# Kernel optimization log

Measured on AMD Instinct MI355X. Metric: run time of the kernel, lower is better.

The kernel has to match this reference:

```python
import math
import jax, jax.numpy as jnp
import numpy as np

B, T, E = 1, 4096, 768
H, D = 12, 64
RA_WINDOW = 512
INIT_GATES = (2.2, 0.6, 0.1)


def setup_inputs() -> dict:
    key = jax.random.key(0)
    ks = jax.random.split(key, 6)
    x = jax.random.normal(ks[0], (B, T, E), dtype=jnp.float32)
    # Linear weights stored as [in, out] (math-equivalent to torch's x @ W.T)
    s = 1.0 / math.sqrt(E)
    Wq = jax.random.normal(ks[1], (E, H * D), dtype=jnp.float32) * s
    Wk = jax.random.normal(ks[2], (E, H * D), dtype=jnp.float32) * s
    Wv = jax.random.normal(ks[3], (E, H * D), dtype=jnp.float32) * s
    Wo = jax.random.normal(ks[4], (H * D, E), dtype=jnp.float32) * s
    gates = jnp.tile(jnp.asarray(INIT_GATES, dtype=jnp.float32)[None, :], (H, 1))  # [H,3]
    u = jax.random.normal(ks[5], (H, D), dtype=jnp.float32) * 0.02
    return {"x": x, "Wq": Wq, "Wk": Wk, "Wv": Wv, "Wo": Wo, "gates": gates, "u": u}


def reference(x, Wq, Wk, Wv, Wo, gates, u):
    # projections -> [B,H,T,D]
    def proj(W):
        return (x @ W).reshape(B, T, H, D).transpose(0, 2, 1, 3)
    Q, K, V = proj(Wq), proj(Wk), proj(Wv)

    S = jnp.einsum('bhtd,bhsd->bhts', Q, K) / math.sqrt(D)  # [B,H,T,T]

    w = jax.nn.softmax(gates, axis=-1)  # [H,3]
    w_std = w[:, 0][None, :, None, None]
    w_rec = w[:, 1][None, :, None, None]
    w_disc = w[:, 2][None, :, None, None]

    logits = w_std * S + w_rec * jnp.swapaxes(S, -2, -1)

    # discoverability column bias from K via per-head u
    d_raw = jnp.einsum('bhtd,hd->bht', K, u)
    d = d_raw - jnp.mean(d_raw, axis=-1, keepdims=True)
    logits = logits + w_disc * d[:, :, None, :]

    # causal banded mask
    idx = jnp.arange(T)
    mask = (idx[None, :] <= idx[:, None]) & (jnp.abs(idx[None, :] - idx[:, None]) <= RA_WINDOW)
    logits = jnp.where(mask[None, None, :, :], logits, -jnp.inf)

    attn = jax.nn.softmax(logits, axis=-1)
    ctx = jnp.einsum('bhts,bhsd->bhtd', attn, V)
    out = ctx.transpose(0, 2, 1, 3).reshape(B, T, H * D) @ Wo
    return (out, attn)
```

## Files before the change

### kernel.cpp

```cpp
#include <hip/hip_runtime.h>
#include <cstddef>

#define T_LEN 4096
#define EMB 768
#define NH 12
#define HD 64
#define WIN 512

__global__ __launch_bounds__(256) void gemm_f32_64x64(const float* __restrict__ A,
                                                      const float* __restrict__ B,
                                                      float* __restrict__ C,
                                                      int M, int N, int K) {
    __shared__ float As[16][68];
    __shared__ float Bs[16][68];
    const int tid = threadIdx.x;
    const int bm = blockIdx.y * 64;
    const int bn = blockIdx.x * 64;
    const int tm = (tid >> 4) << 2;
    const int tn = (tid & 15) << 2;

    const int lm  = tid >> 2;
    const int lk  = (tid & 3) << 2;
    const int bkr = tid >> 4;
    const int bnc = (tid & 15) << 2;

    float acc[4][4] = {};

    for (int k0 = 0; k0 < K; k0 += 16) {
        float4 a4 = *(const float4*)&A[(size_t)(bm + lm) * K + k0 + lk];
        As[lk + 0][lm] = a4.x;
        As[lk + 1][lm] = a4.y;
        As[lk + 2][lm] = a4.z;
        As[lk + 3][lm] = a4.w;
        *(float4*)&Bs[bkr][bnc] = *(const float4*)&B[(size_t)(k0 + bkr) * N + bn + bnc];
        __syncthreads();
#pragma unroll
        for (int k = 0; k < 16; ++k) {
            float4 av = *(float4*)&As[k][tm];
            float4 bv = *(float4*)&Bs[k][tn];
            acc[0][0] += av.x * bv.x; acc[0][1] += av.x * bv.y; acc[0][2] += av.x * bv.z; acc[0][3] += av.x * bv.w;
            acc[1][0] += av.y * bv.x; acc[1][1] += av.y * bv.y; acc[1][2] += av.y * bv.z; acc[1][3] += av.y * bv.w;
            acc[2][0] += av.z * bv.x; acc[2][1] += av.z * bv.y; acc[2][2] += av.z * bv.z; acc[2][3] += av.z * bv.w;
            acc[3][0] += av.w * bv.x; acc[3][1] += av.w * bv.y; acc[3][2] += av.w * bv.z; acc[3][3] += av.w * bv.w;
        }
        __syncthreads();
    }
#pragma unroll
    for (int i = 0; i < 4; ++i) {
        float4 cv = make_float4(acc[i][0], acc[i][1], acc[i][2], acc[i][3]);
        *(float4*)&C[(size_t)(bm + tm + i) * N + bn + tn] = cv;
    }
}

__global__ __launch_bounds__(256) void dbias_kernel(const float* __restrict__ K,
                                                    const float* __restrict__ u,
                                                    float* __restrict__ d_bias) {
    const int h = blockIdx.x;
    const int tid = threadIdx.x;
    __shared__ __align__(16) float us[HD];
    __shared__ float dr[T_LEN];
    __shared__ float red[256];
    if (tid < HD) us[tid] = u[h * HD + tid];
    __syncthreads();
    const float4* u4 = (const float4*)us;
    float lsum = 0.f;
    for (int t = tid; t < T_LEN; t += 256) {
        const float4* Kp = (const float4*)&K[(size_t)t * EMB + h * HD];
        float acc = 0.f;
#pragma unroll
        for (int i = 0; i < HD / 4; ++i) {
            float4 k4 = Kp[i];
            float4 uu = u4[i];
            acc += k4.x * uu.x + k4.y * uu.y + k4.z * uu.z + k4.w * uu.w;
        }
        dr[t] = acc;
        lsum += acc;
    }
    red[tid] = lsum;
    __syncthreads();
    for (int off = 128; off > 0; off >>= 1) {
        if (tid < off) red[tid] += red[tid + off];
        __syncthreads();
    }
    const float mean = red[0] * (1.0f / (float)T_LEN);
    __syncthreads();
    for (int t = tid; t < T_LEN; t += 256) {
        d_bias[h * T_LEN + t] = dr[t] - mean;
    }
}

__global__ __launch_bounds__(256) void attn_band_kernel(const float* __restrict__ Q,
                                                        const float* __restrict__ K,
                                                        const float* __restrict__ V,
                                                        const float* __restrict__ d_bias,
                                                        const float* __restrict__ gates,
                                                        float* __restrict__ attn,
                                                        float* __restrict__ ctx,
                                                        float* __restrict__ row_max,
                                                        float* __restrict__ row_invden) {
    const int t0  = blockIdx.x << 6;
    const int h   = blockIdx.y;
    const int tid = threadIdx.x;
    const int tm  = (tid >> 4) << 2;
    const int tn4 = (tid & 15) << 2;
    const int lm  = tid >> 2;
    const int lk  = (tid & 3) << 2;

    __shared__ __align__(16) float QT[64][68];
    __shared__ __align__(16) float KT[64][68];
    __shared__ __align__(16) float Cc[64][68];
    __shared__ __align__(16) float Vc[64][64];

    const float g0 = gates[h * 3 + 0];
    const float g1 = gates[h * 3 + 1];
    const float g2 = gates[h * 3 + 2];
    const float gm = fmaxf(g0, fmaxf(g1, g2));
    const float e0 = __expf(g0 - gm), e1 = __expf(g1 - gm), e2 = __expf(g2 - gm);
    const float gi = 1.0f / (e0 + e1 + e2);
    const float w_std = e0 * gi * 0.125f;
    const float w_rec = e1 * gi * 0.125f;
    const float w_disc = e2 * gi;

    {
        const float* Qp = Q + (size_t)(t0 + lm) * EMB + h * HD + lk;
        const float* Kp = K + (size_t)(t0 + lm) * EMB + h * HD + lk;
#pragma unroll
        for (int it = 0; it < 4; ++it) {
            float4 a = *(const float4*)(Qp + 16 * it);
            QT[lk + 16 * it + 0][lm] = a.x;
            QT[lk + 16 * it + 1][lm] = a.y;
            QT[lk + 16 * it + 2][lm] = a.z;
            QT[lk + 16 * it + 3][lm] = a.w;
            float4 b = *(const float4*)(Kp + 16 * it);
            KT[lk + 16 * it + 0][lm] = b.x;
            KT[lk + 16 * it + 1][lm] = b.y;
            KT[lk + 16 * it + 2][lm] = b.z;
            KT[lk + 16 * it + 3][lm] = b.w;
        }
    }

    const int s_base = (t0 - WIN > 0) ? (t0 - WIN) : 0;
    const int nch = ((t0 + 64) - s_base) >> 6;

    float rm[4], rden[4], acc[4][4];
#pragma unroll
    for (int i = 0; i < 4; ++i) {
        rm[i] = -1e30f;
        rden[i] = 0.f;
#pragma unroll
        for (int j = 0; j < 4; ++j) acc[i][j] = 0.f;
    }

    for (int c = 0; c < nch; ++c) {
        const int s0 = s_base + (c << 6);
        __syncthreads();
        {
            const float* Kp = K + (size_t)(s0 + lm) * EMB + h * HD + lk;
            const float* Vp = V + (size_t)(s0 + lm) * EMB + h * HD + lk;
#pragma unroll
            for (int it = 0; it < 4; ++it) {
                float4 b = *(const float4*)(Kp + 16 * it);
                Cc[lk + 16 * it + 0][lm] = b.x;
                Cc[lk + 16 * it + 1][lm] = b.y;
                Cc[lk + 16 * it + 2][lm] = b.z;
                Cc[lk + 16 * it + 3][lm] = b.w;
                *(float4*)&Vc[lm][lk + 16 * it] = *(const float4*)(Vp + 16 * it);
            }
        }
        __syncthreads();

        float m1[4][4] = {};
#pragma unroll 16
        for (int k = 0; k < 64; ++k) {
            float4 av = *(const float4*)&QT[k][tm];
            float4 bv = *(const float4*)&Cc[k][tn4];
            m1[0][0] += av.x * bv.x; m1[0][1] += av.x * bv.y; m1[0][2] += av.x * bv.z; m1[0][3] += av.x * bv.w;
            m1[1][0] += av.y * bv.x; m1[1][1] += av.y * bv.y; m1[1][2] += av.y * bv.z; m1[1][3] += av.y * bv.w;
            m1[2][0] += av.z * bv.x; m1[2][1] += av.z * bv.y; m1[2][2] += av.z * bv.z; m1[2][3] += av.z * bv.w;
            m1[3][0] += av.w * bv.x; m1[3][1] += av.w * bv.y; m1[3][2] += av.w * bv.z; m1[3][3] += av.w * bv.w;
        }
        __syncthreads();
        {
            const float* Qp2 = Q + (size_t)(s0 + lm) * EMB + h * HD + lk;
#pragma unroll
            for (int it = 0; it < 4; ++it) {
                float4 b = *(const float4*)(Qp2 + 16 * it);
                Cc[lk + 16 * it + 0][lm] = b.x;
                Cc[lk + 16 * it + 1][lm] = b.y;
                Cc[lk + 16 * it + 2][lm] = b.z;
                Cc[lk + 16 * it + 3][lm] = b.w;
            }
        }
        __syncthreads();

        float m2[4][4] = {};
#pragma unroll 16
        for (int k = 0; k < 64; ++k) {
            float4 av = *(const float4*)&KT[k][tm];
            float4 bv = *(const float4*)&Cc[k][tn4];
            m2[0][0] += av.x * bv.x; m2[0][1] += av.x * bv.y; m2[0][2] += av.x * bv.z; m2[0][3] += av.x * bv.w;
            m2[1][0] += av.y * bv.x; m2[1][1] += av.y * bv.y; m2[1][2] += av.y * bv.z; m2[1][3] += av.y * bv.w;
            m2[2][0] += av.z * bv.x; m2[2][1] += av.z * bv.y; m2[2][2] += av.z * bv.z; m2[2][3] += av.z * bv.w;
            m2[3][0] += av.w * bv.x; m2[3][1] += av.w * bv.y; m2[3][2] += av.w * bv.z; m2[3][3] += av.w * bv.w;
        }

        const float4 db = *(const float4*)&d_bias[h * T_LEN + s0 + tn4];
        float l[4][4];
#pragma unroll
        for (int i = 0; i < 4; ++i) {
            const int t = t0 + tm + i;
            const float dbv[4] = {db.x, db.y, db.z, db.w};
#pragma unroll
            for (int j = 0; j < 4; ++j) {
                const int s = s0 + tn4 + j;
                float lv = w_std * m1[i][j] + w_rec * m2[i][j] + w_disc * dbv[j];
                const bool valid = (s <= t) && (s >= t - WIN);
                l[i][j] = valid ? lv : -1e30f;
            }
            *(float4*)&attn[((size_t)(h * T_LEN + t)) * T_LEN + s0 + tn4] =
                make_float4(l[i][0], l[i][1], l[i][2], l[i][3]);
        }
        float cmx[4];
#pragma unroll
        for (int i = 0; i < 4; ++i)
            cmx[i] = fmaxf(fmaxf(l[i][0], l[i][1]), fmaxf(l[i][2], l[i][3]));
#pragma unroll
        for (int off = 1; off < 16; off <<= 1) {
#pragma unroll
            for (int i = 0; i < 4; ++i) cmx[i] = fmaxf(cmx[i], __shfl_xor(cmx[i], off));
        }
        float cs[4];
#pragma unroll
        for (int i = 0; i < 4; ++i) {
            const float nm = fmaxf(rm[i], cmx[i]);
            const float f = __expf(rm[i] - nm);
            float s = 0.f;
#pragma unroll
            for (int j = 0; j < 4; ++j) {
                const float p = __expf(l[i][j] - nm);
                l[i][j] = p;
                s += p;
            }
            cs[i] = s;
            rm[i] = nm;
            rden[i] *= f;
#pragma unroll
            for (int j = 0; j < 4; ++j) acc[i][j] *= f;
        }
#pragma unroll
        for (int off = 1; off < 16; off <<= 1) {
#pragma unroll
            for (int i = 0; i < 4; ++i) cs[i] += __shfl_xor(cs[i], off);
        }
#pragma unroll
        for (int i = 0; i < 4; ++i) rden[i] += cs[i];

        __syncthreads();
#pragma unroll
        for (int i = 0; i < 4; ++i)
#pragma unroll
            for (int j = 0; j < 4; ++j)
                Cc[tn4 + j][tm + i] = l[i][j];
        __syncthreads();

#pragma unroll 16
        for (int k = 0; k < 64; ++k) {
            float4 av = *(const float4*)&Cc[k][tm];
            float4 bv = *(const float4*)&Vc[k][tn4];
            acc[0][0] += av.x * bv.x; acc[0][1] += av.x * bv.y; acc[0][2] += av.x * bv.z; acc[0][3] += av.x * bv.w;
            acc[1][0] += av.y * bv.x; acc[1][1] += av.y * bv.y; acc[1][2] += av.y * bv.z; acc[1][3] += av.y * bv.w;
            acc[2][0] += av.z * bv.x; acc[2][1] += av.z * bv.y; acc[2][2] += av.z * bv.z; acc[2][3] += av.z * bv.w;
            acc[3][0] += av.w * bv.x; acc[3][1] += av.w * bv.y; acc[3][2] += av.w * bv.z; acc[3][3] += av.w * bv.w;
        }
    }

#pragma unroll
    for (int i = 0; i < 4; ++i) {
        const float idv = 1.0f / rden[i];
        *(float4*)&ctx[(size_t)(t0 + tm + i) * EMB + h * HD + tn4] =
            make_float4(acc[i][0] * idv, acc[i][1] * idv, acc[i][2] * idv, acc[i][3] * idv);
        if ((tid & 15) == 0) {
            row_max[h * T_LEN + t0 + tm + i] = rm[i];
            row_invden[h * T_LEN + t0 + tm + i] = idv;
        }
    }
}

__global__ __launch_bounds__(256) void attn_norm_kernel(float* __restrict__ attn,
                                                        const float* __restrict__ row_max,
                                                        const float* __restrict__ row_invden) {
    const int t = blockIdx.x;
    const int h = blockIdx.y;
    const float m   = row_max[h * T_LEN + t];
    const float idv = row_invden[h * T_LEN + t];
    float* arow = attn + ((size_t)(h * T_LEN + t)) * T_LEN;
    const int bl = (t - WIN > 0) ? (t - WIN) : 0;
    for (int i4 = threadIdx.x << 2; i4 < T_LEN; i4 += 1024) {
        float4 v = make_float4(0.f, 0.f, 0.f, 0.f);
        if (i4 + 3 >= bl && i4 <= t) {
            const float4 r = *(const float4*)&arow[i4];
            v.x = (i4 + 0 >= bl && i4 + 0 <= t) ? __expf(r.x - m) * idv : 0.f;
            v.y = (i4 + 1 >= bl && i4 + 1 <= t) ? __expf(r.y - m) * idv : 0.f;
            v.z = (i4 + 2 >= bl && i4 + 2 <= t) ? __expf(r.z - m) * idv : 0.f;
            v.w = (i4 + 3 >= bl && i4 + 3 <= t) ? __expf(r.w - m) * idv : 0.f;
        }
        *(float4*)&arow[i4] = v;
    }
}

extern "C" void kernel_launch(void* const* d_in, const int* in_sizes, int n_in,
                              void* d_out, int out_size, void* d_ws, size_t ws_size,
                              hipStream_t stream) {
    const float* x     = (const float*)d_in[0];
    const float* Wq    = (const float*)d_in[1];
    const float* Wk    = (const float*)d_in[2];
    const float* Wv    = (const float*)d_in[3];
    const float* Wo    = (const float*)d_in[4];
    const float* gates = (const float*)d_in[5];
    const float* u     = (const float*)d_in[6];

    float* out  = (float*)d_out;
    float* attn = out + (size_t)T_LEN * EMB;

    float* ws = (float*)d_ws;
    float* Qb = ws;
    float* Kb = Qb + (size_t)T_LEN * EMB;
    float* Vb = Kb + (size_t)T_LEN * EMB;
    float* Cb = Vb + (size_t)T_LEN * EMB;
    float* Db = Cb + (size_t)T_LEN * EMB;
    float* Mb = Db + (size_t)NH * T_LEN;
    float* Ib = Mb + (size_t)NH * T_LEN;

    dim3 gg(EMB / 64, T_LEN / 64);
    gemm_f32_64x64<<<gg, 256, 0, stream>>>(x, Wq, Qb, T_LEN, EMB, EMB);
    gemm_f32_64x64<<<gg, 256, 0, stream>>>(x, Wk, Kb, T_LEN, EMB, EMB);
    gemm_f32_64x64<<<gg, 256, 0, stream>>>(x, Wv, Vb, T_LEN, EMB, EMB);
    dbias_kernel<<<NH, 256, 0, stream>>>(Kb, u, Db);

    attn_band_kernel<<<dim3(T_LEN / 64, NH), 256, 0, stream>>>(Qb, Kb, Vb, Db, gates,
                                                               attn, Cb, Mb, Ib);
    attn_norm_kernel<<<dim3(T_LEN, NH), 256, 0, stream>>>(attn, Mb, Ib);

    gemm_f32_64x64<<<gg, 256, 0, stream>>>(Cb, Wo, out, T_LEN, EMB, EMB);
}
```

Baseline: 1.456 ms.

## Batch QKV projections into one 128x128-tiled GEMM and fuse band QK/KQ passes

Replaces the 64x64 GEMM with a 128x128 tile, 8x8-per-thread kernel and launches the Q, K and V projections as a single batched launch over blockIdx.z. The output projection reuses the same kernel. In the band attention kernel, the K and Q chunks are staged together so both score products (QK^T and its transpose) are computed in one k-loop, removing a sync pair and a reload. The V chunk is then loaded into the reused Q buffer. The aim is more arithmetic per shared load and fewer launches and barriers, at the cost of higher register pressure and fewer blocks for the output GEMM.

```diff
diff --git a/kernel.cpp b/kernel.cpp
--- a/kernel.cpp
+++ b/kernel.cpp
@@ -7,48 +7,65 @@
 #define HD 64
 #define WIN 512
 
-__global__ __launch_bounds__(256) void gemm_f32_64x64(const float* __restrict__ A,
-                                                      const float* __restrict__ B,
-                                                      float* __restrict__ C,
-                                                      int M, int N, int K) {
-    __shared__ float As[16][68];
-    __shared__ float Bs[16][68];
+#define GBM 128
+#define GBN 128
+#define GBK 16
+
+__global__ __launch_bounds__(256) void gemm3_f32(const float* __restrict__ A,
+                                                 const float* __restrict__ B0,
+                                                 const float* __restrict__ B1,
+                                                 const float* __restrict__ B2,
+                                                 float* __restrict__ C0,
+                                                 float* __restrict__ C1,
+                                                 float* __restrict__ C2,
+                                                 int M, int N, int K) {
+    __shared__ float As[GBK][GBM + 4];
+    __shared__ float Bs[GBK][GBN + 4];
     const int tid = threadIdx.x;
-    const int bm = blockIdx.y * 64;
-    const int bn = blockIdx.x * 64;
-    const int tm = (tid >> 4) << 2;
-    const int tn = (tid & 15) << 2;
-
-    const int lm  = tid >> 2;
-    const int lk  = (tid & 3) << 2;
-    const int bkr = tid >> 4;
-    const int bnc = (tid & 15) << 2;
-
-    float acc[4][4] = {};
-
-    for (int k0 = 0; k0 < K; k0 += 16) {
-        float4 a4 = *(const float4*)&A[(size_t)(bm + lm) * K + k0 + lk];
-        As[lk + 0][lm] = a4.x;
-        As[lk + 1][lm] = a4.y;
-        As[lk + 2][lm] = a4.z;
-        As[lk + 3][lm] = a4.w;
-        *(float4*)&Bs[bkr][bnc] = *(const float4*)&B[(size_t)(k0 + bkr) * N + bn + bnc];
-        __syncthreads();
-#pragma unroll
-        for (int k = 0; k < 16; ++k) {
-            float4 av = *(float4*)&As[k][tm];
-            float4 bv = *(float4*)&Bs[k][tn];
-            acc[0][0] += av.x * bv.x; acc[0][1] += av.x * bv.y; acc[0][2] += av.x * bv.z; acc[0][3] += av.x * bv.w;
-            acc[1][0] += av.y * bv.x; acc[1][1] += av.y * bv.y; acc[1][2] += av.y * bv.z; acc[1][3] += av.y * bv.w;
-            acc[2][0] += av.z * bv.x; acc[2][1] += av.z * bv.y; acc[2][2] += av.z * bv.z; acc[2][3] += av.z * bv.w;
-            acc[3][0] += av.w * bv.x; acc[3][1] += av.w * bv.y; acc[3][2] += av.w * bv.z; acc[3][3] += av.w * bv.w;
-        }
-        __syncthreads();
-    }
-#pragma unroll
-    for (int i = 0; i < 4; ++i) {
-        float4 cv = make_float4(acc[i][0], acc[i][1], acc[i][2], acc[i][3]);
-        *(float4*)&C[(size_t)(bm + tm + i) * N + bn + tn] = cv;
+    const int bm = blockIdx.y * GBM;
+    const int bn = blockIdx.x * GBN;
+    const float* __restrict__ B = (blockIdx.z == 0) ? B0 : (blockIdx.z == 1) ? B1 : B2;
+    float* __restrict__ C = (blockIdx.z == 0) ? C0 : (blockIdx.z == 1) ? C1 : C2;
+
+    const int ty = (tid >> 4) << 2;
+    const int tx = (tid & 15) << 2;
+
+    const int ar = tid >> 1;
+    const int ac = (tid & 1) << 3;
+    const int br = tid >> 4;
+    const int bc = (tid & 15) << 3;
+
+    float acc[8][8] = {};
+
+    for (int k0 = 0; k0 < K; k0 += GBK) {
+        const float4 a0 = *(const float4*)&A[(size_t)(bm + ar) * K + k0 + ac];
+        const float4 a1 = *(const float4*)&A[(size_t)(bm + ar) * K + k0 + ac + 4];
+        As[ac + 0][ar] = a0.x; As[ac + 1][ar] = a0.y; As[ac + 2][ar] = a0.z; As[ac + 3][ar] = a0.w;
+        As[ac + 4][ar] = a1.x; As[ac + 5][ar] = a1.y; As[ac + 6][ar] = a1.z; As[ac + 7][ar] = a1.w;
+        *(float4*)&Bs[br][bc]     = *(const float4*)&B[(size_t)(k0 + br) * N + bn + bc];
+        *(float4*)&Bs[br][bc + 4] = *(const float4*)&B[(size_t)(k0 + br) * N + bn + bc + 4];
+        __syncthreads();
+#pragma unroll
+        for (int k = 0; k < GBK; ++k) {
+            const float4 a0v = *(const float4*)&As[k][ty];
+            const float4 a1v = *(const float4*)&As[k][ty + 64];
+            const float4 b0v = *(const float4*)&Bs[k][tx];
+            const float4 b1v = *(const float4*)&Bs[k][tx + 64];
+            const float av[8] = {a0v.x, a0v.y, a0v.z, a0v.w, a1v.x, a1v.y, a1v.z, a1v.w};
+            const float bv[8] = {b0v.x, b0v.y, b0v.z, b0v.w, b1v.x, b1v.y, b1v.z, b1v.w};
+#pragma unroll
+            for (int i = 0; i < 8; ++i)
+#pragma unroll
+                for (int j = 0; j < 8; ++j)
+                    acc[i][j] += av[i] * bv[j];
+        }
+        __syncthreads();
+    }
+#pragma unroll
+    for (int i = 0; i < 8; ++i) {
+        const int r = bm + ty + ((i < 4) ? i : (60 + i));
+        *(float4*)&C[(size_t)r * N + bn + tx]      = make_float4(acc[i][0], acc[i][1], acc[i][2], acc[i][3]);
+        *(float4*)&C[(size_t)r * N + bn + tx + 64] = make_float4(acc[i][4], acc[i][5], acc[i][6], acc[i][7]);
     }
 }
 
@@ -109,7 +126,7 @@
     __shared__ __align__(16) float QT[64][68];
     __shared__ __align__(16) float KT[64][68];
     __shared__ __align__(16) float Cc[64][68];
-    __shared__ __align__(16) float Vc[64][64];
+    __shared__ __align__(16) float Qs[64][68];
 
     const float g0 = gates[h * 3 + 0];
     const float g1 = gates[h * 3 + 1];
@@ -156,7 +173,7 @@
         __syncthreads();
         {
             const float* Kp = K + (size_t)(s0 + lm) * EMB + h * HD + lk;
-            const float* Vp = V + (size_t)(s0 + lm) * EMB + h * HD + lk;
+            const float* Qp = Q + (size_t)(s0 + lm) * EMB + h * HD + lk;
 #pragma unroll
             for (int it = 0; it < 4; ++it) {
                 float4 b = *(const float4*)(Kp + 16 * it);
@@ -164,44 +181,31 @@
                 Cc[lk + 16 * it + 1][lm] = b.y;
                 Cc[lk + 16 * it + 2][lm] = b.z;
                 Cc[lk + 16 * it + 3][lm] = b.w;
-                *(float4*)&Vc[lm][lk + 16 * it] = *(const float4*)(Vp + 16 * it);
+                float4 q = *(const float4*)(Qp + 16 * it);
+                Qs[lk + 16 * it + 0][lm] = q.x;
+                Qs[lk + 16 * it + 1][lm] = q.y;
+                Qs[lk + 16 * it + 2][lm] = q.z;
+                Qs[lk + 16 * it + 3][lm] = q.w;
             }
         }
         __syncthreads();
 
         float m1[4][4] = {};
-#pragma unroll 16
+        float m2[4][4] = {};
+#pragma unroll 8
         for (int k = 0; k < 64; ++k) {
-            float4 av = *(const float4*)&QT[k][tm];
-            float4 bv = *(const float4*)&Cc[k][tn4];
-            m1[0][0] += av.x * bv.x; m1[0][1] += av.x * bv.y; m1[0][2] += av.x * bv.z; m1[0][3] += av.x * bv.w;
-            m1[1][0] += av.y * bv.x; m1[1][1] += av.y * bv.y; m1[1][2] += av.y * bv.z; m1[1][3] += av.y * bv.w;
-            m1[2][0] += av.z * bv.x; m1[2][1] += av.z * bv.y; m1[2][2] += av.z * bv.z; m1[2][3] += av.z * bv.w;
-            m1[3][0] += av.w * bv.x; m1[3][1] += av.w * bv.y; m1[3][2] += av.w * bv.z; m1[3][3] += av.w * bv.w;
-        }
-        __syncthreads();
-        {
-            const float* Qp2 = Q + (size_t)(s0 + lm) * EMB + h * HD + lk;
-#pragma unroll
-            for (int it = 0; it < 4; ++it) {
-                float4 b = *(const float4*)(Qp2 + 16 * it);
-                Cc[lk + 16 * it + 0][lm] = b.x;
-                Cc[lk + 16 * it + 1][lm] = b.y;
-                Cc[lk + 16 * it + 2][lm] = b.z;
-                Cc[lk + 16 * it + 3][lm] = b.w;
-            }
-        }
-        __syncthreads();
-
-        float m2[4][4] = {};
-#pragma unroll 16
-        for (int k = 0; k < 64; ++k) {
-            float4 av = *(const float4*)&KT[k][tm];
-            float4 bv = *(const float4*)&Cc[k][tn4];
-            m2[0][0] += av.x * bv.x; m2[0][1] += av.x * bv.y; m2[0][2] += av.x * bv.z; m2[0][3] += av.x * bv.w;
-            m2[1][0] += av.y * bv.x; m2[1][1] += av.y * bv.y; m2[1][2] += av.y * bv.z; m2[1][3] += av.y * bv.w;
-            m2[2][0] += av.z * bv.x; m2[2][1] += av.z * bv.y; m2[2][2] += av.z * bv.z; m2[2][3] += av.z * bv.w;
-            m2[3][0] += av.w * bv.x; m2[3][1] += av.w * bv.y; m2[3][2] += av.w * bv.z; m2[3][3] += av.w * bv.w;
+            const float4 aq = *(const float4*)&QT[k][tm];
+            const float4 bk = *(const float4*)&Cc[k][tn4];
+            const float4 ak = *(const float4*)&KT[k][tm];
+            const float4 bq = *(const float4*)&Qs[k][tn4];
+            m1[0][0] += aq.x * bk.x; m1[0][1] += aq.x * bk.y; m1[0][2] += aq.x * bk.z; m1[0][3] += aq.x * bk.w;
+            m1[1][0] += aq.y * bk.x; m1[1][1] += aq.y * bk.y; m1[1][2] += aq.y * bk.z; m1[1][3] += aq.y * bk.w;
+            m1[2][0] += aq.z * bk.x; m1[2][1] += aq.z * bk.y; m1[2][2] += aq.z * bk.z; m1[2][3] += aq.z * bk.w;
+            m1[3][0] += aq.w * bk.x; m1[3][1] += aq.w * bk.y; m1[3][2] += aq.w * bk.z; m1[3][3] += aq.w * bk.w;
+            m2[0][0] += ak.x * bq.x; m2[0][1] += ak.x * bq.y; m2[0][2] += ak.x * bq.z; m2[0][3] += ak.x * bq.w;
+            m2[1][0] += ak.y * bq.x; m2[1][1] += ak.y * bq.y; m2[1][2] += ak.y * bq.z; m2[1][3] += ak.y * bq.w;
+            m2[2][0] += ak.z * bq.x; m2[2][1] += ak.z * bq.y; m2[2][2] += ak.z * bq.z; m2[2][3] += ak.z * bq.w;
+            m2[3][0] += ak.w * bq.x; m2[3][1] += ak.w * bq.y; m2[3][2] += ak.w * bq.z; m2[3][3] += ak.w * bq.w;
         }
 
         const float4 db = *(const float4*)&d_bias[h * T_LEN + s0 + tn4];
@@ -261,12 +265,18 @@
 #pragma unroll
             for (int j = 0; j < 4; ++j)
                 Cc[tn4 + j][tm + i] = l[i][j];
+        {
+            const float* Vp = V + (size_t)(s0 + lm) * EMB + h * HD + lk;
+#pragma unroll
+            for (int it = 0; it < 4; ++it)
+                *(float4*)&Qs[lm][lk + 16 * it] = *(const float4*)(Vp + 16 * it);
+        }
         __syncthreads();
 
 #pragma unroll 16
         for (int k = 0; k < 64; ++k) {
-            float4 av = *(const float4*)&Cc[k][tm];
-            float4 bv = *(const float4*)&Vc[k][tn4];
+            const float4 av = *(const float4*)&Cc[k][tm];
+            const float4 bv = *(const float4*)&Qs[k][tn4];
             acc[0][0] += av.x * bv.x; acc[0][1] += av.x * bv.y; acc[0][2] += av.x * bv.z; acc[0][3] += av.x * bv.w;
             acc[1][0] += av.y * bv.x; acc[1][1] += av.y * bv.y; acc[1][2] += av.y * bv.z; acc[1][3] += av.y * bv.w;
             acc[2][0] += av.z * bv.x; acc[2][1] += av.z * bv.y; acc[2][2] += av.z * bv.z; acc[2][3] += av.z * bv.w;
@@ -331,15 +341,14 @@
     float* Mb = Db + (size_t)NH * T_LEN;
     float* Ib = Mb + (size_t)NH * T_LEN;
 
-    dim3 gg(EMB / 64, T_LEN / 64);
-    gemm_f32_64x64<<<gg, 256, 0, stream>>>(x, Wq, Qb, T_LEN, EMB, EMB);
-    gemm_f32_64x64<<<gg, 256, 0, stream>>>(x, Wk, Kb, T_LEN, EMB, EMB);
-    gemm_f32_64x64<<<gg, 256, 0, stream>>>(x, Wv, Vb, T_LEN, EMB, EMB);
+    gemm3_f32<<<dim3(EMB / GBN, T_LEN / GBM, 3), 256, 0, stream>>>(
+        x, Wq, Wk, Wv, Qb, Kb, Vb, T_LEN, EMB, EMB);
     dbias_kernel<<<NH, 256, 0, stream>>>(Kb, u, Db);
 
     attn_band_kernel<<<dim3(T_LEN / 64, NH), 256, 0, stream>>>(Qb, Kb, Vb, Db, gates,
                                                                attn, Cb, Mb, Ib);
     attn_norm_kernel<<<dim3(T_LEN, NH), 256, 0, stream>>>(attn, Mb, Ib);
 
-    gemm_f32_64x64<<<gg, 256, 0, stream>>>(Cb, Wo, out, T_LEN, EMB, EMB);
-}
+    gemm3_f32<<<dim3(EMB / GBN, T_LEN / GBM, 1), 256, 0, stream>>>(
+        Cb, Wo, Wo, Wo, out, out, out, T_LEN, EMB, EMB);
+}
```

Measured after the change: 1.459 ms. Within noise of the previous version (+0.2%).
